# Kernel optimization log

Hardware: AMD Instinct MI355X
Metric: run time of the kernel (lower is better)

## Reference

```python
import jax, jax.numpy as jnp
import numpy as np

N_NODES = 100000
N_EDGES = 20000
NNZ = 1600000


def _hconv(x, W, b, node_idx, edge_idx):
    # torch-geometric HypergraphConv, no attention, hyperedge_weight = 1
    x = x @ W                                                   # [N, F_out]
    ones = jnp.ones((NNZ,), dtype=x.dtype)
    deg_e = jax.ops.segment_sum(ones, edge_idx, num_segments=N_EDGES)   # |e|
    deg_n = jax.ops.segment_sum(ones, node_idx, num_segments=N_NODES)   # node degree
    B = jnp.where(deg_e > 0, 1.0 / deg_e, 0.0)
    D = jnp.where(deg_n > 0, 1.0 / deg_n, 0.0)
    # node -> edge: e_feat[e] = B_e * sum_{i in e} x_i
    e_feat = B[:, None] * jax.ops.segment_sum(x[node_idx], edge_idx, num_segments=N_EDGES)
    # edge -> node: out[i] = D_i * sum_{e ni i} e_feat[e]
    out = D[:, None] * jax.ops.segment_sum(e_feat[edge_idx], node_idx, num_segments=N_NODES)
    return out + b


def setup_inputs() -> dict:
    key = jax.random.key(0)
    ks = jax.random.split(key, 9)
    x = jax.random.normal(ks[0], (N_NODES, 128), dtype=jnp.float32)
    node_idx = jax.random.randint(ks[1], (NNZ,), 0, N_NODES, dtype=jnp.int64 if jax.config.jax_enable_x64 else jnp.int32)
    edge_idx = jax.random.randint(ks[2], (NNZ,), 0, N_EDGES, dtype=jnp.int64 if jax.config.jax_enable_x64 else jnp.int32)
    def lin(k, fi, fo):
        s = 1.0 / np.sqrt(fi)
        return jax.random.uniform(k, (fi, fo), jnp.float32, -s, s)
    W1 = lin(ks[3], 128, 128); b1 = jnp.zeros((128,), jnp.float32)
    W2 = lin(ks[4], 128, 128); b2 = jnp.zeros((128,), jnp.float32)
    W3 = lin(ks[5], 128, 64);  b3 = jnp.zeros((64,), jnp.float32)
    return {"x": x, "W1": W1, "b1": b1, "W2": W2, "b2": b2, "W3": W3, "b3": b3,
            "node_idx": node_idx, "edge_idx": edge_idx}


def reference(x, W1, b1, W2, b2, W3, b3, node_idx, edge_idx):
    h = _hconv(x, W1, b1, node_idx, edge_idx)
    h = jax.nn.relu(h)          # dropout p=0 -> identity
    h = _hconv(h, W2, b2, node_idx, edge_idx)
    h = jax.nn.relu(h)
    h = _hconv(h, W3, b3, node_idx, edge_idx)
    return h
```

## Files before the change

### kernel.cpp

```cpp
#include <hip/hip_runtime.h>

#define N_NODES 100000
#define N_EDGES 20000
#define NNZV    1600000
#define NSEG    (N_EDGES + N_NODES)
#define FIN     128
#define NPART   8
#define E_PER_P (N_EDGES / NPART)
#define N_PER_P (N_NODES / NPART)
#define HSLICES 32

__device__ __forceinline__ unsigned short f2bf(float f) {
  unsigned u = __float_as_uint(f);
  unsigned r = u + 0x7fffu + ((u >> 16) & 1u);
  return (unsigned short)(r >> 16);
}
__device__ __forceinline__ unsigned pack2(float lo, float hi) {
  return (unsigned)f2bf(lo) | ((unsigned)f2bf(hi) << 16);
}
__device__ __forceinline__ float bf_lo(unsigned w) { return __uint_as_float(w << 16); }
__device__ __forceinline__ float bf_hi(unsigned w) { return __uint_as_float(w & 0xffff0000u); }


__global__ __launch_bounds__(256) void k_hist(const int* __restrict__ nidx,
                                              const int* __restrict__ eidx,
                                              int* __restrict__ part) {
  __shared__ int hist[12544];
  int r = blockIdx.x % 10, s = blockIdx.x / 10;
  const int* arr; int base, size, bin_off;
  if (r < 2) { arr = eidx; base = r * 10000; size = 10000; bin_off = r * 10000; }
  else { int ri = r - 2; arr = nidx; base = ri * N_PER_P; size = N_PER_P; bin_off = N_EDGES + ri * N_PER_P; }
  for (int i = threadIdx.x; i < size; i += 256) hist[i] = 0;
  __syncthreads();
  int lo = s * (NNZV / HSLICES), hi = lo + (NNZV / HSLICES);
  for (int i = lo + threadIdx.x; i < hi; i += 256) {
    int v = __builtin_nontemporal_load(arr + i);
    unsigned d = (unsigned)(v - base);
    if (d < (unsigned)size) atomicAdd(&hist[d], 1);
  }
  __syncthreads();
  int* dst = part + (size_t)s * NSEG + bin_off;
  for (int i = threadIdx.x; i < size; i += 256) dst[i] = hist[i];
}

__global__ void k_hreduce(const int* __restrict__ part, int* __restrict__ cnt) {
  int b = blockIdx.x * 256 + threadIdx.x;
  if (b >= NSEG) return;
  int sum = 0;
#pragma unroll
  for (int s = 0; s < HSLICES; ++s) sum += part[(size_t)s * NSEG + b];
  cnt[b] = sum;
}


__global__ void k_scan1(const int* __restrict__ cnt, int* __restrict__ incl,
                        int* __restrict__ bsum) {
  __shared__ int s[1024];
  int gid = blockIdx.x * 1024 + threadIdx.x;
  int v = (gid < NSEG) ? cnt[gid] : 0;
  s[threadIdx.x] = v;
  __syncthreads();
  for (int d = 1; d < 1024; d <<= 1) {
    int t = (threadIdx.x >= d) ? s[threadIdx.x - d] : 0;
    __syncthreads();
    s[threadIdx.x] += t;
    __syncthreads();
  }
  if (gid < NSEG) incl[gid] = s[threadIdx.x];
  if (threadIdx.x == 1023) bsum[blockIdx.x] = s[1023];
}

__global__ void k_scan2(int* __restrict__ bsum, int nb) {
  __shared__ int s[128];
  int v = (threadIdx.x < nb) ? bsum[threadIdx.x] : 0;
  s[threadIdx.x] = v;
  __syncthreads();
  for (int d = 1; d < 128; d <<= 1) {
    int t = (threadIdx.x >= (unsigned)d) ? s[threadIdx.x - d] : 0;
    __syncthreads();
    s[threadIdx.x] += t;
    __syncthreads();
  }
  if (threadIdx.x < nb) bsum[threadIdx.x] = s[threadIdx.x] - v;
}

__global__ void k_scan3(int* __restrict__ off, const int* __restrict__ cnt,
                        const int* __restrict__ bsum) {
  int gid = blockIdx.x * 1024 + threadIdx.x;
  if (gid < NSEG) off[gid] = off[gid] - cnt[gid] + bsum[blockIdx.x];
}


__global__ void k_fill(const int* __restrict__ nidx, const int* __restrict__ eidx,
                       const int* __restrict__ off, int* __restrict__ cur,
                       int* __restrict__ csr) {
  int p = blockIdx.x & (NPART - 1);
  int e_lo = p * E_PER_P, e_hi = e_lo + E_PER_P;
  int n_lo = p * N_PER_P, n_hi = n_lo + N_PER_P;
  int i = (blockIdx.x >> 3) * blockDim.x + threadIdx.x;
  int st = (gridDim.x >> 3) * blockDim.x;
  for (; i < NNZV; i += st) {
    int e = __builtin_nontemporal_load(eidx + i);
    int n = __builtin_nontemporal_load(nidx + i);
    if (e >= e_lo && e < e_hi) {
      int pe = atomicAdd(&cur[e], 1);
      csr[off[e] + pe] = n;
    }
    if (n >= n_lo && n < n_hi) {
      int pn = atomicAdd(&cur[N_EDGES + n], 1);
      csr[off[N_EDGES + n] + pn] = e;
    }
  }
}


__global__ void k_tobf(const float2* __restrict__ x2, unsigned* __restrict__ xbf) {
  int t = blockIdx.x * 256 + threadIdx.x;
  float2 v = x2[t];
  xbf[t] = pack2(v.x, v.y);
}


__global__ __launch_bounds__(256) void k_passAbf(const unsigned* __restrict__ tab,
                                                 const int* __restrict__ csr,
                                                 const int* __restrict__ off,
                                                 const int* __restrict__ cnt,
                                                 float* __restrict__ ebuf) {
  int wave = (blockIdx.x * blockDim.x + threadIdx.x) >> 6;
  int lane = threadIdx.x & 63;
  if (wave >= N_EDGES) return;
  int beg = off[wave];
  int m   = cnt[wave];
  const unsigned* src = tab + lane;
  float accx = 0.f, accy = 0.f;
  int idxv = 0;
  int j = 0;
  for (; j + 8 <= m; j += 8) {
    int jm = j & 63;
    if (jm == 0) {
      int p = j + lane;
      idxv = (p < m) ? __builtin_nontemporal_load(csr + beg + p) : 0;
    }
    int n0 = __shfl(idxv, jm);
    int n1 = __shfl(idxv, jm + 1);
    int n2 = __shfl(idxv, jm + 2);
    int n3 = __shfl(idxv, jm + 3);
    int n4 = __shfl(idxv, jm + 4);
    int n5 = __shfl(idxv, jm + 5);
    int n6 = __shfl(idxv, jm + 6);
    int n7 = __shfl(idxv, jm + 7);
    unsigned w0 = src[(size_t)n0 * 64];
    unsigned w1 = src[(size_t)n1 * 64];
    unsigned w2 = src[(size_t)n2 * 64];
    unsigned w3 = src[(size_t)n3 * 64];
    unsigned w4 = src[(size_t)n4 * 64];
    unsigned w5 = src[(size_t)n5 * 64];
    unsigned w6 = src[(size_t)n6 * 64];
    unsigned w7 = src[(size_t)n7 * 64];
    accx += ((bf_lo(w0) + bf_lo(w1)) + (bf_lo(w2) + bf_lo(w3))) +
            ((bf_lo(w4) + bf_lo(w5)) + (bf_lo(w6) + bf_lo(w7)));
    accy += ((bf_hi(w0) + bf_hi(w1)) + (bf_hi(w2) + bf_hi(w3))) +
            ((bf_hi(w4) + bf_hi(w5)) + (bf_hi(w6) + bf_hi(w7)));
  }
  for (; j < m; ++j) {
    int jm = j & 63;
    if (jm == 0) {
      int p = j + lane;
      idxv = (p < m) ? __builtin_nontemporal_load(csr + beg + p) : 0;
    }
    int n0 = __shfl(idxv, jm);
    unsigned w = src[(size_t)n0 * 64];
    accx += bf_lo(w); accy += bf_hi(w);
  }
  float binv = (m > 0) ? (1.f / (float)m) : 0.f;
  *reinterpret_cast<float2*>(ebuf + (size_t)wave * FIN + lane * 2) =
      make_float2(accx * binv, accy * binv);
}


__global__ void k_gemm128b(const float* __restrict__ A, const float* __restrict__ W,
                           unsigned* __restrict__ Out) {
  __shared__ float As[64][33];
  __shared__ float Ws[32][128];
  int tid = threadIdx.x;
  int tx = tid % 16, ty = tid / 16;
  int row0 = blockIdx.x * 64;
  float acc[4][8];
#pragma unroll
  for (int i = 0; i < 4; ++i)
#pragma unroll
    for (int j = 0; j < 8; ++j) acc[i][j] = 0.f;

  for (int kc = 0; kc < FIN; kc += 32) {
    for (int i = tid; i < 64 * 32; i += 256) {
      int r = i >> 5, k = i & 31;
      int gr = row0 + r;
      As[r][k] = (gr < N_EDGES) ? A[(size_t)gr * FIN + kc + k] : 0.f;
    }
    for (int i = tid; i < 32 * 128; i += 256) {
      int k = i >> 7, cc = i & 127;
      Ws[k][cc] = W[(size_t)(kc + k) * 128 + cc];
    }
    __syncthreads();
#pragma unroll
    for (int k = 0; k < 32; ++k) {
      float a[4];
#pragma unroll
      for (int i = 0; i < 4; ++i) a[i] = As[ty * 4 + i][k];
      float w[8];
#pragma unroll
      for (int j = 0; j < 8; ++j) w[j] = Ws[k][tx * 8 + j];
#pragma unroll
      for (int i = 0; i < 4; ++i)
#pragma unroll
        for (int j = 0; j < 8; ++j) acc[i][j] += a[i] * w[j];
    }
    __syncthreads();
  }
#pragma unroll
  for (int i = 0; i < 4; ++i) {
    int gr = row0 + ty * 4 + i;
    if (gr < N_EDGES) {
#pragma unroll
      for (int jj = 0; jj < 4; ++jj)
        Out[(size_t)gr * 64 + tx * 4 + jj] = pack2(acc[i][2 * jj], acc[i][2 * jj + 1]);
    }
  }
}


template <bool RELU>
__global__ __launch_bounds__(256) void k_passBbf(const unsigned* __restrict__ tab,
                                                 const int* __restrict__ csr,
                                                 const int* __restrict__ off,
                                                 const int* __restrict__ cnt,
                                                 const float* __restrict__ bias,
                                                 unsigned* __restrict__ hbf) {
  int wave = (blockIdx.x * blockDim.x + threadIdx.x) >> 6;
  int lane = threadIdx.x & 63;
  if (wave >= N_NODES) return;
  int beg = off[N_EDGES + wave];
  int m   = cnt[N_EDGES + wave];
  const unsigned* src = tab + lane;
  float accx = 0.f, accy = 0.f;
  int idxv = 0;
  int j = 0;
  for (; j + 8 <= m; j += 8) {
    int jm = j & 63;
    if (jm == 0) {
      int p = j + lane;
      idxv = (p < m) ? __builtin_nontemporal_load(csr + beg + p) : 0;
    }
    int n0 = __shfl(idxv, jm);
    int n1 = __shfl(idxv, jm + 1);
    int n2 = __shfl(idxv, jm + 2);
    int n3 = __shfl(idxv, jm + 3);
    int n4 = __shfl(idxv, jm + 4);
    int n5 = __shfl(idxv, jm + 5);
    int n6 = __shfl(idxv, jm + 6);
    int n7 = __shfl(idxv, jm + 7);
    unsigned w0 = src[(size_t)n0 * 64];
    unsigned w1 = src[(size_t)n1 * 64];
    unsigned w2 = src[(size_t)n2 * 64];
    unsigned w3 = src[(size_t)n3 * 64];
    unsigned w4 = src[(size_t)n4 * 64];
    unsigned w5 = src[(size_t)n5 * 64];
    unsigned w6 = src[(size_t)n6 * 64];
    unsigned w7 = src[(size_t)n7 * 64];
    accx += ((bf_lo(w0) + bf_lo(w1)) + (bf_lo(w2) + bf_lo(w3))) +
            ((bf_lo(w4) + bf_lo(w5)) + (bf_lo(w6) + bf_lo(w7)));
    accy += ((bf_hi(w0) + bf_hi(w1)) + (bf_hi(w2) + bf_hi(w3))) +
            ((bf_hi(w4) + bf_hi(w5)) + (bf_hi(w6) + bf_hi(w7)));
  }
  for (; j < m; ++j) {
    int jm = j & 63;
    if (jm == 0) {
      int p = j + lane;
      idxv = (p < m) ? __builtin_nontemporal_load(csr + beg + p) : 0;
    }
    int n0 = __shfl(idxv, jm);
    unsigned w = src[(size_t)n0 * 64];
    accx += bf_lo(w); accy += bf_hi(w);
  }
  float dinv = (m > 0) ? (1.f / (float)m) : 0.f;
  float ox = accx * dinv + bias[lane * 2];
  float oy = accy * dinv + bias[lane * 2 + 1];
  if (RELU) { ox = fmaxf(ox, 0.f); oy = fmaxf(oy, 0.f); }
  hbf[(size_t)wave * 64 + lane] = pack2(ox, oy);
}


__global__ void k_gemm_node_b(const unsigned* __restrict__ hbf, const float* __restrict__ W,
                              unsigned* __restrict__ Out) {
  __shared__ float As[64][33];
  __shared__ float Ws[32][64];
  int tid = threadIdx.x;
  int tx = tid % 8, ty = tid / 8;
  int row0 = blockIdx.x * 64;
  float acc[4][8];
#pragma unroll
  for (int i = 0; i < 4; ++i)
#pragma unroll
    for (int j = 0; j < 8; ++j) acc[i][j] = 0.f;

  for (int kc = 0; kc < FIN; kc += 32) {
    for (int i = tid; i < 64 * 16; i += 128) {
      int r = i >> 4, kp = i & 15;
      int gr = row0 + r;
      unsigned w = (gr < N_NODES) ? hbf[(size_t)gr * 64 + (kc >> 1) + kp] : 0u;
      As[r][2 * kp]     = bf_lo(w);
      As[r][2 * kp + 1] = bf_hi(w);
    }
    for (int i = tid; i < 32 * 64; i += 128) {
      int k = i >> 6, cc = i & 63;
      Ws[k][cc] = W[(size_t)(kc + k) * 64 + cc];
    }
    __syncthreads();
#pragma unroll
    for (int k = 0; k < 32; ++k) {
      float a[4];
#pragma unroll
      for (int i = 0; i < 4; ++i) a[i] = As[ty * 4 + i][k];
      float w[8];
#pragma unroll
      for (int j = 0; j < 8; ++j) w[j] = Ws[k][tx * 8 + j];
#pragma unroll
      for (int i = 0; i < 4; ++i)
#pragma unroll
        for (int j = 0; j < 8; ++j) acc[i][j] += a[i] * w[j];
    }
    __syncthreads();
  }
#pragma unroll
  for (int i = 0; i < 4; ++i) {
    int gr = row0 + ty * 4 + i;
    if (gr < N_NODES) {
#pragma unroll
      for (int jj = 0; jj < 4; ++jj)
        Out[(size_t)gr * 32 + tx * 4 + jj] = pack2(acc[i][2 * jj], acc[i][2 * jj + 1]);
    }
  }
}


__global__ __launch_bounds__(256) void k_passA64b(const unsigned short* __restrict__ tab,
                                                  const int* __restrict__ csr,
                                                  const int* __restrict__ off,
                                                  const int* __restrict__ cnt,
                                                  unsigned short* __restrict__ eb3) {
  int wave = (blockIdx.x * blockDim.x + threadIdx.x) >> 6;
  int lane = threadIdx.x & 63;
  if (wave >= N_EDGES) return;
  int beg = off[wave];
  int m   = cnt[wave];
  const unsigned short* src = tab + lane;
  float acc = 0.f;
  int idxv = 0;
  int j = 0;
  for (; j + 8 <= m; j += 8) {
    int jm = j & 63;
    if (jm == 0) {
      int p = j + lane;
      idxv = (p < m) ? __builtin_nontemporal_load(csr + beg + p) : 0;
    }
    int n0 = __shfl(idxv, jm);
    int n1 = __shfl(idxv, jm + 1);
    int n2 = __shfl(idxv, jm + 2);
    int n3 = __shfl(idxv, jm + 3);
    int n4 = __shfl(idxv, jm + 4);
    int n5 = __shfl(idxv, jm + 5);
    int n6 = __shfl(idxv, jm + 6);
    int n7 = __shfl(idxv, jm + 7);
    float v0 = __uint_as_float((unsigned)src[(size_t)n0 * 64] << 16);
    float v1 = __uint_as_float((unsigned)src[(size_t)n1 * 64] << 16);
    float v2 = __uint_as_float((unsigned)src[(size_t)n2 * 64] << 16);
    float v3 = __uint_as_float((unsigned)src[(size_t)n3 * 64] << 16);
    float v4 = __uint_as_float((unsigned)src[(size_t)n4 * 64] << 16);
    float v5 = __uint_as_float((unsigned)src[(size_t)n5 * 64] << 16);
    float v6 = __uint_as_float((unsigned)src[(size_t)n6 * 64] << 16);
    float v7 = __uint_as_float((unsigned)src[(size_t)n7 * 64] << 16);
    acc += ((v0 + v1) + (v2 + v3)) + ((v4 + v5) + (v6 + v7));
  }
  for (; j < m; ++j) {
    int jm = j & 63;
    if (jm == 0) {
      int p = j + lane;
      idxv = (p < m) ? __builtin_nontemporal_load(csr + beg + p) : 0;
    }
    int n0 = __shfl(idxv, jm);
    acc += __uint_as_float((unsigned)src[(size_t)n0 * 64] << 16);
  }
  float binv = (m > 0) ? (1.f / (float)m) : 0.f;
  eb3[(size_t)wave * 64 + lane] = f2bf(acc * binv);
}


__global__ __launch_bounds__(256) void k_passB64b(const unsigned short* __restrict__ tab,
                                                  const int* __restrict__ csr,
                                                  const int* __restrict__ off,
                                                  const int* __restrict__ cnt,
                                                  const float* __restrict__ bias,
                                                  float* __restrict__ out) {
  int wave = (blockIdx.x * blockDim.x + threadIdx.x) >> 6;
  int lane = threadIdx.x & 63;
  if (wave >= N_NODES) return;
  int beg = off[N_EDGES + wave];
  int m   = cnt[N_EDGES + wave];
  const unsigned short* src = tab + lane;
  float acc = 0.f;
  int idxv = 0;
  int j = 0;
  for (; j + 8 <= m; j += 8) {
    int jm = j & 63;
    if (jm == 0) {
      int p = j + lane;
      idxv = (p < m) ? __builtin_nontemporal_load(csr + beg + p) : 0;
    }
    int n0 = __shfl(idxv, jm);
    int n1 = __shfl(idxv, jm + 1);
    int n2 = __shfl(idxv, jm + 2);
    int n3 = __shfl(idxv, jm + 3);
    int n4 = __shfl(idxv, jm + 4);
    int n5 = __shfl(idxv, jm + 5);
    int n6 = __shfl(idxv, jm + 6);
    int n7 = __shfl(idxv, jm + 7);
    float v0 = __uint_as_float((unsigned)src[(size_t)n0 * 64] << 16);
    float v1 = __uint_as_float((unsigned)src[(size_t)n1 * 64] << 16);
    float v2 = __uint_as_float((unsigned)src[(size_t)n2 * 64] << 16);
    float v3 = __uint_as_float((unsigned)src[(size_t)n3 * 64] << 16);
    float v4 = __uint_as_float((unsigned)src[(size_t)n4 * 64] << 16);
    float v5 = __uint_as_float((unsigned)src[(size_t)n5 * 64] << 16);
    float v6 = __uint_as_float((unsigned)src[(size_t)n6 * 64] << 16);
    float v7 = __uint_as_float((unsigned)src[(size_t)n7 * 64] << 16);
    acc += ((v0 + v1) + (v2 + v3)) + ((v4 + v5) + (v6 + v7));
  }
  for (; j < m; ++j) {
    int jm = j & 63;
    if (jm == 0) {
      int p = j + lane;
      idxv = (p < m) ? __builtin_nontemporal_load(csr + beg + p) : 0;
    }
    int n0 = __shfl(idxv, jm);
    acc += __uint_as_float((unsigned)src[(size_t)n0 * 64] << 16);
  }
  float dinv = (m > 0) ? (1.f / (float)m) : 0.f;
  out[(size_t)wave * 64 + lane] = acc * dinv + bias[lane];
}


extern "C" void kernel_launch(void* const* d_in, const int* in_sizes, int n_in,
                              void* d_out, int out_size, void* d_ws, size_t ws_size,
                              hipStream_t stream) {
  const float* x  = (const float*)d_in[0];
  const float* W1 = (const float*)d_in[1];
  const float* b1 = (const float*)d_in[2];
  const float* W2 = (const float*)d_in[3];
  const float* b2 = (const float*)d_in[4];
  const float* W3 = (const float*)d_in[5];
  const float* b3 = (const float*)d_in[6];
  const int* nidx = (const int*)d_in[7];
  const int* eidx = (const int*)d_in[8];

  const size_t OFF_CNT  = 0;
  const size_t OFF_OFF  = 480000;
  const size_t OFF_CUR  = 960000;
  const size_t OFF_BSUM = 1440000;
  const size_t OFF_CSR  = 1441792;
  const size_t OFF_EB   = 14241792;
  const size_t OFF_EB2  = 24481792;
  const size_t OFF_XBF  = 29601792;
  const size_t OFF_HBF  = 55201792;
  const size_t NEEDED   = 80801792;
  if (ws_size < NEEDED) return;

  char* ws = (char*)d_ws;
  int*      cnt   = (int*)(ws + OFF_CNT);
  int*      off   = (int*)(ws + OFF_OFF);
  int*      cur   = (int*)(ws + OFF_CUR);
  int*      bsum  = (int*)(ws + OFF_BSUM);
  int*      csr   = (int*)(ws + OFF_CSR);
  int*      part  = (int*)(ws + OFF_EB);
  float*    ebuf  = (float*)(ws + OFF_EB);
  unsigned* eb2bf = (unsigned*)(ws + OFF_EB2);
  unsigned* xbf   = (unsigned*)(ws + OFF_XBF);
  unsigned* hw3   = (unsigned*)(ws + OFF_XBF);
  unsigned short* eb3 = (unsigned short*)(ws + OFF_EB);
  unsigned* hbf   = (unsigned*)(ws + OFF_HBF);
  float*    out   = (float*)d_out;

  hipMemsetAsync(ws + OFF_CUR, 0, 480512, stream);

  k_hist<<<10 * HSLICES, 256, 0, stream>>>(nidx, eidx, part);
  k_hreduce<<<(NSEG + 255) / 256, 256, 0, stream>>>(part, cnt);
  const int nb = (NSEG + 1023) / 1024;
  k_scan1<<<nb, 1024, 0, stream>>>(cnt, off, bsum);
  k_scan2<<<1, 128, 0, stream>>>(bsum, nb);
  k_scan3<<<nb, 1024, 0, stream>>>(off, cnt, bsum);
  k_fill<<<1024, 256, 0, stream>>>(nidx, eidx, off, cur, csr);

  k_tobf<<<25000, 256, 0, stream>>>((const float2*)x, xbf);

  const int BLK_A = (N_EDGES * 64 + 255) / 256;
  const int BLK_B = (N_NODES * 64 + 255) / 256;
  const int BLK_G = (N_EDGES + 63) / 64;
  const int BLK_GN = (N_NODES + 63) / 64;

  k_passAbf<<<BLK_A, 256, 0, stream>>>(xbf, csr, off, cnt, ebuf);
  k_gemm128b<<<BLK_G, 256, 0, stream>>>(ebuf, W1, eb2bf);
  k_passBbf<true><<<BLK_B, 256, 0, stream>>>(eb2bf, csr, off, cnt, b1, hbf);

  k_passAbf<<<BLK_A, 256, 0, stream>>>(hbf, csr, off, cnt, ebuf);
  k_gemm128b<<<BLK_G, 256, 0, stream>>>(ebuf, W2, eb2bf);
  k_passBbf<true><<<BLK_B, 256, 0, stream>>>(eb2bf, csr, off, cnt, b2, hbf);

  k_gemm_node_b<<<BLK_GN, 128, 0, stream>>>(hbf, W3, hw3);
  k_passA64b<<<BLK_A, 256, 0, stream>>>((const unsigned short*)hw3, csr, off, cnt, eb3);
  k_passB64b<<<BLK_B, 256, 0, stream>>>(eb3, csr, off, cnt, b3, out);
}
```

Baseline: 726.8 us.

## Build CSR with per-slice histogram bases and shared-memory ranks instead of global atomics

Reuses the per-slice histogram counts to compute each slice's starting offset per segment, then fills the CSR with blocks that rank entries through shared-memory atomics. This replaces the global atomic cursor array and its memset. The aim is to cut global atomic contention and the repeated scans over the index arrays during CSR construction. It adds one extra kernel pass over the partial histograms.

```diff
diff --git a/kernel.cpp b/kernel.cpp
--- a/kernel.cpp
+++ b/kernel.cpp
@@ -5,9 +5,7 @@
 #define NNZV    1600000
 #define NSEG    (N_EDGES + N_NODES)
 #define FIN     128
-#define NPART   8
-#define E_PER_P (N_EDGES / NPART)
-#define N_PER_P (N_NODES / NPART)
+#define N_PER_P (N_NODES / 8)
 #define HSLICES 32
 
 __device__ __forceinline__ unsigned short f2bf(float f) {
@@ -91,24 +89,42 @@
 }
 
 
-__global__ void k_fill(const int* __restrict__ nidx, const int* __restrict__ eidx,
-                       const int* __restrict__ off, int* __restrict__ cur,
-                       int* __restrict__ csr) {
-  int p = blockIdx.x & (NPART - 1);
-  int e_lo = p * E_PER_P, e_hi = e_lo + E_PER_P;
-  int n_lo = p * N_PER_P, n_hi = n_lo + N_PER_P;
-  int i = (blockIdx.x >> 3) * blockDim.x + threadIdx.x;
-  int st = (gridDim.x >> 3) * blockDim.x;
-  for (; i < NNZV; i += st) {
-    int e = __builtin_nontemporal_load(eidx + i);
-    int n = __builtin_nontemporal_load(nidx + i);
-    if (e >= e_lo && e < e_hi) {
-      int pe = atomicAdd(&cur[e], 1);
-      csr[off[e] + pe] = n;
-    }
-    if (n >= n_lo && n < n_hi) {
-      int pn = atomicAdd(&cur[N_EDGES + n], 1);
-      csr[off[N_EDGES + n] + pn] = e;
+__global__ void k_sbase(int* __restrict__ part, const int* __restrict__ off) {
+  int b = blockIdx.x * 256 + threadIdx.x;
+  if (b >= NSEG) return;
+  int running = off[b];
+#pragma unroll
+  for (int s = 0; s < HSLICES; ++s) {
+    size_t idx = (size_t)s * NSEG + b;
+    int t = part[idx];
+    part[idx] = running;
+    running += t;
+  }
+}
+
+
+__global__ __launch_bounds__(256) void k_fill2(const int* __restrict__ nidx,
+                                               const int* __restrict__ eidx,
+                                               const int* __restrict__ sbase,
+                                               int* __restrict__ csr) {
+  __shared__ int rank[12544];
+  int r = blockIdx.x % 10, s = blockIdx.x / 10;
+  int base, size, bin_off; bool er;
+  if (r < 2) { base = r * 10000; size = 10000; bin_off = 0; er = true; }
+  else { base = (r - 2) * N_PER_P; size = N_PER_P; bin_off = N_EDGES; er = false; }
+  for (int i = threadIdx.x; i < size; i += 256) rank[i] = 0;
+  __syncthreads();
+  int lo = s * (NNZV / HSLICES), hi = lo + (NNZV / HSLICES);
+  const int* keys = er ? eidx : nidx;
+  const int* vals = er ? nidx : eidx;
+  const int* sb = sbase + (size_t)s * NSEG + bin_off;
+  for (int i = lo + threadIdx.x; i < hi; i += 256) {
+    int k = __builtin_nontemporal_load(keys + i);
+    int v = __builtin_nontemporal_load(vals + i);
+    unsigned d = (unsigned)(k - base);
+    if (d < (unsigned)size) {
+      int rk = atomicAdd(&rank[d], 1);
+      csr[sb[k] + rk] = v;
     }
   }
 }
@@ -463,7 +479,6 @@
 
   const size_t OFF_CNT  = 0;
   const size_t OFF_OFF  = 480000;
-  const size_t OFF_CUR  = 960000;
   const size_t OFF_BSUM = 1440000;
   const size_t OFF_CSR  = 1441792;
   const size_t OFF_EB   = 14241792;
@@ -476,7 +491,6 @@
   char* ws = (char*)d_ws;
   int*      cnt   = (int*)(ws + OFF_CNT);
   int*      off   = (int*)(ws + OFF_OFF);
-  int*      cur   = (int*)(ws + OFF_CUR);
   int*      bsum  = (int*)(ws + OFF_BSUM);
   int*      csr   = (int*)(ws + OFF_CSR);
   int*      part  = (int*)(ws + OFF_EB);
@@ -488,7 +502,7 @@
   unsigned* hbf   = (unsigned*)(ws + OFF_HBF);
   float*    out   = (float*)d_out;
 
-  hipMemsetAsync(ws + OFF_CUR, 0, 480512, stream);
+  hipMemsetAsync(ws + OFF_BSUM, 0, 512, stream);
 
   k_hist<<<10 * HSLICES, 256, 0, stream>>>(nidx, eidx, part);
   k_hreduce<<<(NSEG + 255) / 256, 256, 0, stream>>>(part, cnt);
@@ -496,7 +510,8 @@
   k_scan1<<<nb, 1024, 0, stream>>>(cnt, off, bsum);
   k_scan2<<<1, 128, 0, stream>>>(bsum, nb);
   k_scan3<<<nb, 1024, 0, stream>>>(off, cnt, bsum);
-  k_fill<<<1024, 256, 0, stream>>>(nidx, eidx, off, cur, csr);
+  k_sbase<<<(NSEG + 255) / 256, 256, 0, stream>>>(part, off);
+  k_fill2<<<10 * HSLICES, 256, 0, stream>>>(nidx, eidx, part, csr);
 
   k_tobf<<<25000, 256, 0, stream>>>((const float2*)x, xbf);
 
```

After: 829.9 us. 1.14x slower.
